# Performance work log

Hardware: AMD Instinct MI355X
Metric: run time of the kernel (lower is better)

## Reference

```python
import jax, jax.numpy as jnp
import numpy as np

N, E, FN, FE, L, G = 4096, 16384, 16, 8, 128, 64
EPS = 1e-5


def setup_inputs() -> dict:
    key = jax.random.key(0)
    ks = iter(jax.random.split(key, 40))

    def lin_w(shape):
        return jax.random.normal(next(ks), shape, jnp.float32) * (1.0 / np.sqrt(shape[0]))

    d = {}
    d["x"] = jax.random.normal(next(ks), (N, FN), jnp.float32)
    d["edge_attr"] = jax.random.normal(next(ks), (E, FE), jnp.float32)
    d["edge_index"] = jax.random.randint(next(ks), (2, E), 0, N)
    d["batch"] = jnp.sort(jax.random.randint(next(ks), (N,), 0, G))
    for i, (cin, cout) in enumerate([(FN, 32), (32, 64), (64, 128)], 1):
        d[f"We{i}"] = lin_w((FE, cin * cout))          # edge_fc weight
        d[f"be{i}"] = jnp.zeros((cin * cout,), jnp.float32)
        d[f"bias{i}"] = jnp.zeros((cout,), jnp.float32)
        d[f"Wr{i}"] = lin_w((cin, cout))               # res_fc weight
        d[f"br{i}"] = jnp.zeros((cout,), jnp.float32)
        d[f"bn_g{i}"] = jnp.ones((cout,), jnp.float32)
        d[f"bn_b{i}"] = jnp.zeros((cout,), jnp.float32)
        d[f"a{i}"] = jnp.float32(0.25)                  # PReLU slope
    d["Wi"] = lin_w((128, 128)); d["bi"] = jnp.zeros((128,), jnp.float32)
    d["Wj"] = lin_w((128, 128)); d["bj"] = jnp.zeros((128,), jnp.float32)
    d["Wfc"] = lin_w((128, 2 * L)); d["bfc"] = jnp.zeros((2 * L,), jnp.float32)
    return d


def _ecc(x, src, dst, norm, edge_attr, We, be, bias, Wr, br, cout, cin):
    # dynamically generated per-edge filter: [E, out, in]
    theta = (edge_attr @ We + be).reshape(E, cout, cin)
    # gather source features, per-edge matvec, degree-normalize (norm_j)
    msg = norm[src][:, None] * jnp.einsum('eoi,ei->eo', theta, x[src])
    # scatter-add into destination nodes + bias + residual linear
    return jax.ops.segment_sum(msg, dst, num_segments=N) + bias + x @ Wr + br


def _bn(x, g, b):
    m = x.mean(0)
    v = x.var(0)  # biased variance, as torch BN training normalization
    return (x - m) * jax.lax.rsqrt(v + EPS) * g + b


def _prelu(x, a):
    return jnp.where(x >= 0, x, a * x)


def reference(x, edge_attr, edge_index, batch,
              We1, be1, bias1, Wr1, br1, bn_g1, bn_b1, a1,
              We2, be2, bias2, Wr2, br2, bn_g2, bn_b2, a2,
              We3, be3, bias3, Wr3, br3, bn_g3, bn_b3, a3,
              Wi, bi, Wj, bj, Wfc, bfc):
    src, dst = edge_index[0], edge_index[1]
    deg = jax.ops.segment_sum(jnp.ones((E,), x.dtype), src, num_segments=N)
    norm = jnp.where(deg > 0, 1.0 / deg, 0.0)

    h = _ecc(x, src, dst, norm, edge_attr, We1, be1, bias1, Wr1, br1, 32, FN)
    h = _prelu(_bn(h, bn_g1, bn_b1), a1)
    h = _ecc(h, src, dst, norm, edge_attr, We2, be2, bias2, Wr2, br2, 64, 32)
    h = _prelu(_bn(h, bn_g2, bn_b2), a2)
    h = _ecc(h, src, dst, norm, edge_attr, We3, be3, bias3, Wr3, br3, 128, 64)
    h = _prelu(_bn(h, bn_g3, bn_b3), a3)

    # gated attention pooling (GGS-NN eq. 7), scatter-sum per graph
    gates = jax.nn.sigmoid(h @ Wi + bi)
    feats = jnp.tanh(h @ Wj + bj)
    pooled = jnp.tanh(jax.ops.segment_sum(gates * feats, batch, num_segments=G))

    z = pooled @ Wfc + bfc  # [G, 2L]
    return z[:, :L], z[:, L:]
```

## Files before the change

### kernel.cpp

```cpp
#include <hip/hip_runtime.h>
#include <math.h>

#define NN 4096
#define NE 16384
#define NG 64

#define OFF_DEG   0
#define OFF_H1    4096
#define OFF_H2    135168
#define OFF_H3    397312
#define OFF_ST1   921600
#define OFF_ST2   921664
#define OFF_ST3   921792
#define OFF_POOL  922048
#define OFF_WET1  930240
#define OFF_BET1  934336
#define OFF_WET2  934848
#define OFF_BET2  951232
#define OFF_WET3  953280
#define OFF_BET3  1018816
#define ZERO_FLOATS 930240

__device__ __forceinline__ void tr_we(const float* We, float* WeT, int CIN, int COUT, int t) {
    int per = CIN * COUT;
    int f = t / per; int r = t - f * per;
    int o = r / CIN; int i = r - o * CIN;
    WeT[(f * CIN + i) * COUT + o] = We[t];
}
__device__ __forceinline__ void tr_be(const float* be, float* beT, int CIN, int COUT, int t) {
    int o = t / CIN; int i = t - o * CIN;
    beT[i * COUT + o] = be[t];
}

__global__ __launch_bounds__(256) void k_prep(
    const float* __restrict__ We1, const float* __restrict__ be1,
    const float* __restrict__ We2, const float* __restrict__ be2,
    const float* __restrict__ We3, const float* __restrict__ be3,
    const int* __restrict__ ei, float* __restrict__ ws)
{
    int t = blockIdx.x * 256 + threadIdx.x;
    if (t < 4096)  { tr_we(We1, ws + OFF_WET1, 16, 32, t); return; }
    t -= 4096;
    if (t < 512)   { tr_be(be1, ws + OFF_BET1, 16, 32, t); return; }
    t -= 512;
    if (t < 16384) { tr_we(We2, ws + OFF_WET2, 32, 64, t); return; }
    t -= 16384;
    if (t < 2048)  { tr_be(be2, ws + OFF_BET2, 32, 64, t); return; }
    t -= 2048;
    if (t < 65536) { tr_we(We3, ws + OFF_WET3, 64, 128, t); return; }
    t -= 65536;
    if (t < 8192)  { tr_be(be3, ws + OFF_BET3, 64, 128, t); return; }
    t -= 8192;
    if (t < NE)    { atomicAdd(&ws[OFF_DEG + ei[t]], 1.0f); }
}

template<int CIN, int COUT, int TO, int EL, int KE>
__global__ __launch_bounds__(TO*EL) void k_edge(
    const float* __restrict__ xin, const float* __restrict__ eattr,
    const int* __restrict__ ei, const float* __restrict__ deg,
    const float* __restrict__ WeT, const float* __restrict__ beT,
    float* __restrict__ hout)
{
    constexpr int TE = EL * KE;
    constexpr int NT = TO * EL;
    constexpr int CINP = CIN | 1;
    __shared__ float sWe[8 * CIN * TO];
    __shared__ float sBe[CIN * TO];
    __shared__ float sX[TE * CINP];
    __shared__ float sEa[TE * 8];
    __shared__ float sNorm[TE];
    __shared__ int   sDst[TE];
    const int tid = threadIdx.x;
    const int ebase = blockIdx.x * TE;
    const int obase = blockIdx.y * TO;

    for (int t = tid; t < 8 * CIN * TO; t += NT) {
        int fi = t / TO, o = t % TO;
        sWe[t] = WeT[fi * COUT + obase + o];
    }
    for (int t = tid; t < CIN * TO; t += NT) {
        int i = t / TO, o = t % TO;
        sBe[t] = beT[i * COUT + obase + o];
    }
    for (int t = tid; t < TE * CIN; t += NT) {
        int el = t / CIN, i = t % CIN;
        int s = ei[ebase + el];
        sX[el * CINP + i] = xin[s * CIN + i];
    }
    for (int t = tid; t < TE * 8; t += NT) sEa[t] = eattr[ebase * 8 + t];
    if (tid < TE) {
        int s = ei[ebase + tid];
        float d = deg[s];
        sNorm[tid] = d > 0.f ? 1.f / d : 0.f;
        sDst[tid] = ei[NE + ebase + tid];
    }
    __syncthreads();

    const int o  = tid % TO;
    const int el = tid / TO;

    float ea[KE][8];
#pragma unroll
    for (int k = 0; k < KE; ++k)
#pragma unroll
        for (int f = 0; f < 8; ++f)
            ea[k][f] = sEa[(el * KE + k) * 8 + f];

    float acc[KE];
#pragma unroll
    for (int k = 0; k < KE; ++k) acc[k] = 0.f;

    for (int i = 0; i < CIN; ++i) {
        float w[8];
#pragma unroll
        for (int f = 0; f < 8; ++f) w[f] = sWe[(f * CIN + i) * TO + o];
        float bw = sBe[i * TO + o];
#pragma unroll
        for (int k = 0; k < KE; ++k) {
            float th = bw;
#pragma unroll
            for (int f = 0; f < 8; ++f) th += ea[k][f] * w[f];
            acc[k] += th * sX[(el * KE + k) * CINP + i];
        }
    }
#pragma unroll
    for (int k = 0; k < KE; ++k) {
        int e = el * KE + k;
        atomicAdd(&hout[sDst[e] * COUT + obase + o], acc[k] * sNorm[e]);
    }
}

template<int CIN, int COUT, int KN>
__global__ __launch_bounds__(256) void k_node(
    const float* __restrict__ xin, const float* __restrict__ Wr,
    const float* __restrict__ br, const float* __restrict__ bias,
    float* __restrict__ h, float* __restrict__ st)
{
    constexpr int NL = 256 / COUT;
    constexpr int NB = NL * KN;
    constexpr int CINP = CIN | 1;
    __shared__ float sWr[CIN * COUT];
    __shared__ float sX[NB * CINP];
    __shared__ float sred[256];
    const int tid = threadIdx.x;
    const int nbase = blockIdx.x * NB;

    for (int t = tid; t < CIN * COUT; t += 256) sWr[t] = Wr[t];
    for (int t = tid; t < NB * CIN; t += 256) {
        int r = t / CIN, i = t % CIN;
        sX[r * CINP + i] = xin[(nbase + r) * CIN + i];
    }
    __syncthreads();

    const int o = tid % COUT;
    const int nl = tid / COUT;
    const float addc = bias[o] + br[o];
    float sum = 0.f, sumsq = 0.f;
    for (int k = 0; k < KN; ++k) {
        int r = nl * KN + k;
        float a = addc;
        for (int i = 0; i < CIN; ++i)
            a += sX[r * CINP + i] * sWr[i * COUT + o];
        int gi = (nbase + r) * COUT + o;
        float hv = h[gi] + a;
        h[gi] = hv;
        sum += hv; sumsq += hv * hv;
    }
    sred[tid] = sum;
    __syncthreads();
    if (tid < COUT) {
        float s = 0.f;
        for (int g2 = 0; g2 < NL; ++g2) s += sred[g2 * COUT + tid];
        atomicAdd(&st[tid], s);
    }
    __syncthreads();
    sred[tid] = sumsq;
    __syncthreads();
    if (tid < COUT) {
        float s = 0.f;
        for (int g2 = 0; g2 < NL; ++g2) s += sred[g2 * COUT + tid];
        atomicAdd(&st[COUT + tid], s);
    }
}

template<int COUT>
__global__ __launch_bounds__(256) void k_bn(
    float* __restrict__ h, const float* __restrict__ st,
    const float* __restrict__ g, const float* __restrict__ b,
    const float* __restrict__ a)
{
    int idx = blockIdx.x * 256 + threadIdx.x;
    int o = idx % COUT;
    float mean = st[o] * (1.f / NN);
    float var = st[COUT + o] * (1.f / NN) - mean * mean;
    var = fmaxf(var, 0.f);
    float inv = rsqrtf(var + 1e-5f);
    float v = (h[idx] - mean) * inv * g[o] + b[o];
    h[idx] = v >= 0.f ? v : a[0] * v;
}

__global__ __launch_bounds__(256) void k_pool(
    const float* __restrict__ h3, const int* __restrict__ batch,
    const float* __restrict__ Wi, const float* __restrict__ bi,
    const float* __restrict__ Wj, const float* __restrict__ bj,
    float* __restrict__ pooled)
{
    constexpr int KN = 8, NB = 16;
    __shared__ float sH[NB * 128];
    __shared__ int sB[NB];
    const int tid = threadIdx.x;
    const int nbase = blockIdx.x * NB;
    for (int t = tid; t < NB * 128; t += 256) sH[t] = h3[nbase * 128 + t];
    if (tid < NB) sB[tid] = batch[nbase + tid];
    __syncthreads();

    const int o = tid % 128, nl = tid / 128;
    float gacc[KN], facc[KN];
#pragma unroll
    for (int k = 0; k < KN; ++k) { gacc[k] = 0.f; facc[k] = 0.f; }
    for (int i = 0; i < 128; ++i) {
        float wi = Wi[i * 128 + o], wj = Wj[i * 128 + o];
#pragma unroll
        for (int k = 0; k < KN; ++k) {
            float hv = sH[(nl * KN + k) * 128 + i];
            gacc[k] += hv * wi;
            facc[k] += hv * wj;
        }
    }
    float bio = bi[o], bjo = bj[o];
#pragma unroll
    for (int k = 0; k < KN; ++k) {
        int r = nl * KN + k;
        float gate = 1.f / (1.f + expf(-(gacc[k] + bio)));
        float feat = tanhf(facc[k] + bjo);
        atomicAdd(&pooled[sB[r] * 128 + o], gate * feat);
    }
}

__global__ __launch_bounds__(256) void k_final(
    const float* __restrict__ pooled, const float* __restrict__ Wfc,
    const float* __restrict__ bfc, float* __restrict__ out)
{
    __shared__ float sP[128];
    const int g = blockIdx.x, c = threadIdx.x;
    if (c < 128) sP[c] = tanhf(pooled[g * 128 + c]);
    __syncthreads();
    float z = bfc[c];
    for (int i = 0; i < 128; ++i) z += sP[i] * Wfc[i * 256 + c];
    int oidx = (c < 128) ? (g * 128 + c) : (NG * 128 + g * 128 + (c - 128));
    out[oidx] = z;
}

extern "C" void kernel_launch(void* const* d_in, const int* in_sizes, int n_in,
                              void* d_out, int out_size, void* d_ws, size_t ws_size,
                              hipStream_t stream)
{
    (void)in_sizes; (void)n_in; (void)out_size; (void)ws_size;
    const float* x     = (const float*)d_in[0];
    const float* eattr = (const float*)d_in[1];
    const int*   ei    = (const int*)d_in[2];
    const int*   batch = (const int*)d_in[3];
    const float* We1 = (const float*)d_in[4];
    const float* be1 = (const float*)d_in[5];
    const float* bias1 = (const float*)d_in[6];
    const float* Wr1 = (const float*)d_in[7];
    const float* br1 = (const float*)d_in[8];
    const float* bg1 = (const float*)d_in[9];
    const float* bb1 = (const float*)d_in[10];
    const float* a1  = (const float*)d_in[11];
    const float* We2 = (const float*)d_in[12];
    const float* be2 = (const float*)d_in[13];
    const float* bias2 = (const float*)d_in[14];
    const float* Wr2 = (const float*)d_in[15];
    const float* br2 = (const float*)d_in[16];
    const float* bg2 = (const float*)d_in[17];
    const float* bb2 = (const float*)d_in[18];
    const float* a2  = (const float*)d_in[19];
    const float* We3 = (const float*)d_in[20];
    const float* be3 = (const float*)d_in[21];
    const float* bias3 = (const float*)d_in[22];
    const float* Wr3 = (const float*)d_in[23];
    const float* br3 = (const float*)d_in[24];
    const float* bg3 = (const float*)d_in[25];
    const float* bb3 = (const float*)d_in[26];
    const float* a3  = (const float*)d_in[27];
    const float* Wi  = (const float*)d_in[28];
    const float* bi  = (const float*)d_in[29];
    const float* Wj  = (const float*)d_in[30];
    const float* bj  = (const float*)d_in[31];
    const float* Wfc = (const float*)d_in[32];
    const float* bfc = (const float*)d_in[33];
    float* ws  = (float*)d_ws;
    float* out = (float*)d_out;

    hipMemsetAsync(d_ws, 0, (size_t)ZERO_FLOATS * sizeof(float), stream);
    k_prep<<<442, 256, 0, stream>>>(We1, be1, We2, be2, We3, be3, ei, ws);

    k_edge<16, 32, 32, 8, 8><<<dim3(NE / 64, 1), 256, 0, stream>>>(
        x, eattr, ei, ws + OFF_DEG, ws + OFF_WET1, ws + OFF_BET1, ws + OFF_H1);
    k_node<16, 32, 8><<<NN / 64, 256, 0, stream>>>(x, Wr1, br1, bias1, ws + OFF_H1, ws + OFF_ST1);
    k_bn<32><<<NN * 32 / 256, 256, 0, stream>>>(ws + OFF_H1, ws + OFF_ST1, bg1, bb1, a1);

    k_edge<32, 64, 32, 8, 8><<<dim3(NE / 64, 2), 256, 0, stream>>>(
        ws + OFF_H1, eattr, ei, ws + OFF_DEG, ws + OFF_WET2, ws + OFF_BET2, ws + OFF_H2);
    k_node<32, 64, 8><<<NN / 32, 256, 0, stream>>>(ws + OFF_H1, Wr2, br2, bias2, ws + OFF_H2, ws + OFF_ST2);
    k_bn<64><<<NN * 64 / 256, 256, 0, stream>>>(ws + OFF_H2, ws + OFF_ST2, bg2, bb2, a2);

    k_edge<64, 128, 16, 16, 4><<<dim3(NE / 64, 8), 256, 0, stream>>>(
        ws + OFF_H2, eattr, ei, ws + OFF_DEG, ws + OFF_WET3, ws + OFF_BET3, ws + OFF_H3);
    k_node<64, 128, 8><<<NN / 16, 256, 0, stream>>>(ws + OFF_H2, Wr3, br3, bias3, ws + OFF_H3, ws + OFF_ST3);
    k_bn<128><<<NN * 128 / 256, 256, 0, stream>>>(ws + OFF_H3, ws + OFF_ST3, bg3, bb3, a3);

    k_pool<<<NN / 16, 256, 0, stream>>>(ws + OFF_H3, batch, Wi, bi, Wj, bj, ws + OFF_POOL);
    k_final<<<NG, 256, 0, stream>>>(ws + OFF_POOL, Wfc, bfc, out);
}
```

Baseline: 286.1 us.

## Factor edge-conditioned conv into per-node projection GEMM plus edge gather

```diff
diff --git a/kernel.cpp b/kernel.cpp
--- a/kernel.cpp
+++ b/kernel.cpp
@@ -13,23 +13,18 @@
 #define OFF_ST2   921664
 #define OFF_ST3   921792
 #define OFF_POOL  922048
-#define OFF_WET1  930240
-#define OFF_BET1  934336
-#define OFF_WET2  934848
-#define OFF_BET2  951232
-#define OFF_WET3  953280
-#define OFF_BET3  1018816
+#define OFF_WC1   930240
+#define OFF_WC2   934848
+#define OFF_WC3   953280
+#define OFF_Y     1027008
 #define ZERO_FLOATS 930240
 
-__device__ __forceinline__ void tr_we(const float* We, float* WeT, int CIN, int COUT, int t) {
-    int per = CIN * COUT;
-    int f = t / per; int r = t - f * per;
-    int o = r / CIN; int i = r - o * CIN;
-    WeT[(f * CIN + i) * COUT + o] = We[t];
-}
-__device__ __forceinline__ void tr_be(const float* be, float* beT, int CIN, int COUT, int t) {
-    int o = t / CIN; int i = t - o * CIN;
-    beT[i * COUT + o] = be[t];
+__device__ __forceinline__ void tr_wcat(const float* We, const float* be,
+                                        float* Wcat, int CIN, int COUT, int t) {
+    int nine = 9 * COUT;
+    int i = t / nine; int r = t - i * nine;
+    int f = r / COUT; int o = r - f * COUT;
+    Wcat[t] = (f < 8) ? We[f * CIN * COUT + o * CIN + i] : be[o * CIN + i];
 }
 
 __global__ __launch_bounds__(256) void k_prep(
@@ -39,95 +34,79 @@
     const int* __restrict__ ei, float* __restrict__ ws)
 {
     int t = blockIdx.x * 256 + threadIdx.x;
-    if (t < 4096)  { tr_we(We1, ws + OFF_WET1, 16, 32, t); return; }
-    t -= 4096;
-    if (t < 512)   { tr_be(be1, ws + OFF_BET1, 16, 32, t); return; }
-    t -= 512;
-    if (t < 16384) { tr_we(We2, ws + OFF_WET2, 32, 64, t); return; }
-    t -= 16384;
-    if (t < 2048)  { tr_be(be2, ws + OFF_BET2, 32, 64, t); return; }
-    t -= 2048;
-    if (t < 65536) { tr_we(We3, ws + OFF_WET3, 64, 128, t); return; }
-    t -= 65536;
-    if (t < 8192)  { tr_be(be3, ws + OFF_BET3, 64, 128, t); return; }
-    t -= 8192;
+    if (t < 4608)  { tr_wcat(We1, be1, ws + OFF_WC1, 16, 32, t); return; }
+    t -= 4608;
+    if (t < 18432) { tr_wcat(We2, be2, ws + OFF_WC2, 32, 64, t); return; }
+    t -= 18432;
+    if (t < 73728) { tr_wcat(We3, be3, ws + OFF_WC3, 64, 128, t); return; }
+    t -= 73728;
     if (t < NE)    { atomicAdd(&ws[OFF_DEG + ei[t]], 1.0f); }
 }
 
-template<int CIN, int COUT, int TO, int EL, int KE>
-__global__ __launch_bounds__(TO*EL) void k_edge(
-    const float* __restrict__ xin, const float* __restrict__ eattr,
-    const int* __restrict__ ei, const float* __restrict__ deg,
-    const float* __restrict__ WeT, const float* __restrict__ beT,
-    float* __restrict__ hout)
-{
-    constexpr int TE = EL * KE;
-    constexpr int NT = TO * EL;
-    constexpr int CINP = CIN | 1;
-    __shared__ float sWe[8 * CIN * TO];
-    __shared__ float sBe[CIN * TO];
-    __shared__ float sX[TE * CINP];
-    __shared__ float sEa[TE * 8];
-    __shared__ float sNorm[TE];
-    __shared__ int   sDst[TE];
+template<int K>
+__global__ __launch_bounds__(256) void k_proj(
+    const float* __restrict__ A,
+    const float* __restrict__ B,
+    const float* __restrict__ deg,
+    float* __restrict__ Y, int Ncols)
+{
+    __shared__ float sA[K][68];
+    __shared__ float sB[K][68];
     const int tid = threadIdx.x;
-    const int ebase = blockIdx.x * TE;
-    const int obase = blockIdx.y * TO;
-
-    for (int t = tid; t < 8 * CIN * TO; t += NT) {
-        int fi = t / TO, o = t % TO;
-        sWe[t] = WeT[fi * COUT + obase + o];
-    }
-    for (int t = tid; t < CIN * TO; t += NT) {
-        int i = t / TO, o = t % TO;
-        sBe[t] = beT[i * COUT + obase + o];
-    }
-    for (int t = tid; t < TE * CIN; t += NT) {
-        int el = t / CIN, i = t % CIN;
-        int s = ei[ebase + el];
-        sX[el * CINP + i] = xin[s * CIN + i];
-    }
-    for (int t = tid; t < TE * 8; t += NT) sEa[t] = eattr[ebase * 8 + t];
-    if (tid < TE) {
-        int s = ei[ebase + tid];
-        float d = deg[s];
-        sNorm[tid] = d > 0.f ? 1.f / d : 0.f;
-        sDst[tid] = ei[NE + ebase + tid];
-    }
-    __syncthreads();
-
-    const int o  = tid % TO;
-    const int el = tid / TO;
-
-    float ea[KE][8];
-#pragma unroll
-    for (int k = 0; k < KE; ++k)
-#pragma unroll
-        for (int f = 0; f < 8; ++f)
-            ea[k][f] = sEa[(el * KE + k) * 8 + f];
-
-    float acc[KE];
-#pragma unroll
-    for (int k = 0; k < KE; ++k) acc[k] = 0.f;
-
-    for (int i = 0; i < CIN; ++i) {
-        float w[8];
-#pragma unroll
-        for (int f = 0; f < 8; ++f) w[f] = sWe[(f * CIN + i) * TO + o];
-        float bw = sBe[i * TO + o];
-#pragma unroll
-        for (int k = 0; k < KE; ++k) {
-            float th = bw;
-#pragma unroll
-            for (int f = 0; f < 8; ++f) th += ea[k][f] * w[f];
-            acc[k] += th * sX[(el * KE + k) * CINP + i];
+    const int m0 = blockIdx.x * 64;
+    const int n0 = blockIdx.y * 64;
+
+    for (int t = tid; t < 64 * K; t += 256) {
+        int m = t / K, i = t - m * K;
+        sA[i][m] = A[(m0 + m) * K + i];
+    }
+    for (int t = tid; t < 64 * K; t += 256) {
+        int i = t / 64, n = t - i * 64;
+        int col = n0 + n;
+        sB[i][n] = (col < Ncols) ? B[i * Ncols + col] : 0.f;
+    }
+    __syncthreads();
+
+    const int tn = tid % 16, tm = tid / 16;
+    float acc[4][4] = {{0.f}};
+#pragma unroll 8
+    for (int i = 0; i < K; ++i) {
+        float4 a = *(const float4*)&sA[i][tm * 4];
+        float4 b = *(const float4*)&sB[i][tn * 4];
+        acc[0][0] += a.x * b.x; acc[0][1] += a.x * b.y; acc[0][2] += a.x * b.z; acc[0][3] += a.x * b.w;
+        acc[1][0] += a.y * b.x; acc[1][1] += a.y * b.y; acc[1][2] += a.y * b.z; acc[1][3] += a.y * b.w;
+        acc[2][0] += a.z * b.x; acc[2][1] += a.z * b.y; acc[2][2] += a.z * b.z; acc[2][3] += a.z * b.w;
+        acc[3][0] += a.w * b.x; acc[3][1] += a.w * b.y; acc[3][2] += a.w * b.z; acc[3][3] += a.w * b.w;
+    }
+
+#pragma unroll
+    for (int mm = 0; mm < 4; ++mm) {
+        int m = m0 + tm * 4 + mm;
+        float d = deg[m];
+        float nrm = d > 0.f ? 1.f / d : 0.f;
+#pragma unroll
+        for (int nn = 0; nn < 4; ++nn) {
+            int col = n0 + tn * 4 + nn;
+            if (col < Ncols) Y[(size_t)m * Ncols + col] = acc[mm][nn] * nrm;
         }
     }
-#pragma unroll
-    for (int k = 0; k < KE; ++k) {
-        int e = el * KE + k;
-        atomicAdd(&hout[sDst[e] * COUT + obase + o], acc[k] * sNorm[e]);
-    }
+}
+
+template<int COUT>
+__global__ __launch_bounds__(256) void k_egather(
+    const float* __restrict__ Y, const float* __restrict__ eattr,
+    const int* __restrict__ ei, float* __restrict__ h)
+{
+    int idx = blockIdx.x * 256 + threadIdx.x;
+    int e = idx / COUT;
+    int o = idx - e * COUT;
+    int src = ei[e], dst = ei[NE + e];
+    const float* y = Y + (size_t)src * (9 * COUT);
+    const float* ea = eattr + e * 8;
+    float acc = y[8 * COUT + o];
+#pragma unroll
+    for (int f = 0; f < 8; ++f) acc += ea[f] * y[f * COUT + o];
+    atomicAdd(&h[dst * COUT + o], acc);
 }
 
 template<int CIN, int COUT, int KN>
@@ -147,7 +126,7 @@
 
     for (int t = tid; t < CIN * COUT; t += 256) sWr[t] = Wr[t];
     for (int t = tid; t < NB * CIN; t += 256) {
-        int r = t / CIN, i = t % CIN;
+        int r = t / CIN, i = t - r * CIN;
         sX[r * CINP + i] = xin[(nbase + r) * CIN + i];
     }
     __syncthreads();
@@ -296,18 +275,18 @@
     hipMemsetAsync(d_ws, 0, (size_t)ZERO_FLOATS * sizeof(float), stream);
     k_prep<<<442, 256, 0, stream>>>(We1, be1, We2, be2, We3, be3, ei, ws);
 
-    k_edge<16, 32, 32, 8, 8><<<dim3(NE / 64, 1), 256, 0, stream>>>(
-        x, eattr, ei, ws + OFF_DEG, ws + OFF_WET1, ws + OFF_BET1, ws + OFF_H1);
+    k_proj<16><<<dim3(64, 5), 256, 0, stream>>>(x, ws + OFF_WC1, ws + OFF_DEG, ws + OFF_Y, 288);
+    k_egather<32><<<NE * 32 / 256, 256, 0, stream>>>(ws + OFF_Y, eattr, ei, ws + OFF_H1);
     k_node<16, 32, 8><<<NN / 64, 256, 0, stream>>>(x, Wr1, br1, bias1, ws + OFF_H1, ws + OFF_ST1);
     k_bn<32><<<NN * 32 / 256, 256, 0, stream>>>(ws + OFF_H1, ws + OFF_ST1, bg1, bb1, a1);
 
-    k_edge<32, 64, 32, 8, 8><<<dim3(NE / 64, 2), 256, 0, stream>>>(
-        ws + OFF_H1, eattr, ei, ws + OFF_DEG, ws + OFF_WET2, ws + OFF_BET2, ws + OFF_H2);
+    k_proj<32><<<dim3(64, 9), 256, 0, stream>>>(ws + OFF_H1, ws + OFF_WC2, ws + OFF_DEG, ws + OFF_Y, 576);
+    k_egather<64><<<NE * 64 / 256, 256, 0, stream>>>(ws + OFF_Y, eattr, ei, ws + OFF_H2);
     k_node<32, 64, 8><<<NN / 32, 256, 0, stream>>>(ws + OFF_H1, Wr2, br2, bias2, ws + OFF_H2, ws + OFF_ST2);
     k_bn<64><<<NN * 64 / 256, 256, 0, stream>>>(ws + OFF_H2, ws + OFF_ST2, bg2, bb2, a2);
 
-    k_edge<64, 128, 16, 16, 4><<<dim3(NE / 64, 8), 256, 0, stream>>>(
-        ws + OFF_H2, eattr, ei, ws + OFF_DEG, ws + OFF_WET3, ws + OFF_BET3, ws + OFF_H3);
+    k_proj<64><<<dim3(64, 18), 256, 0, stream>>>(ws + OFF_H2, ws + OFF_WC3, ws + OFF_DEG, ws + OFF_Y, 1152);
+    k_egather<128><<<NE * 128 / 256, 256, 0, stream>>>(ws + OFF_Y, eattr, ei, ws + OFF_H3);
     k_node<64, 128, 8><<<NN / 16, 256, 0, stream>>>(ws + OFF_H2, Wr3, br3, bias3, ws + OFF_H3, ws + OFF_ST3);
     k_bn<128><<<NN * 128 / 256, 256, 0, stream>>>(ws + OFF_H3, ws + OFF_ST3, bg3, bb3, a3);
 
```

After: 255.9 us. -10.5%, faster.
